# Kernel tuning notes

Measured on AMD Instinct MI355X. Metric: run time of the kernel, lower is better.

## Reference

```python
import jax, jax.numpy as jnp
import numpy as np

B, S, H, NH = 2, 2048, 1024, 16
HD = H // NH  # head_dim = 64


def setup_inputs() -> dict:
    key = jax.random.key(0)
    k1, k2, k3 = jax.random.split(key, 3)
    x = jax.random.normal(k1, (B, S, H), dtype=jnp.float32)
    # additive causal mask: 0 on/below diagonal, -1e9 above
    causal = jnp.tril(jnp.ones((S, S), dtype=bool))
    mask = jnp.where(causal, 0.0, -1e9).astype(jnp.float32)[None, None, :, :]
    # fan-in scaled init like flax Dense default (lecun_normal)
    W_qkv = jax.random.normal(k2, (H, 3 * H), dtype=jnp.float32) / np.sqrt(H)
    W_out = jax.random.normal(k3, (H, H), dtype=jnp.float32) / np.sqrt(H)
    return {"x": x, "mask": mask, "W_qkv": W_qkv, "W_out": W_out}


def reference(x, mask, W_qkv, W_out):
    b, s, _ = x.shape
    qkv = jnp.einsum('bsh,hf->bsf', x, W_qkv)  # [B,S,3H]
    q, k, v = jnp.split(qkv, 3, axis=-1)
    q = q.reshape(b, s, NH, HD)
    k = k.reshape(b, s, NH, HD)
    v = v.reshape(b, s, NH, HD)
    scores = jnp.einsum('bqhd,bkhd->bhqk', q, k) / jnp.sqrt(jnp.float32(HD))
    scores = scores + mask
    attn = jax.nn.softmax(scores, axis=-1)
    y = jnp.einsum('bhqk,bkhd->bqhd', attn, v).reshape(b, s, H)
    return jnp.einsum('bsh,ho->bso', y, W_out)
```

## Files before the change

### kernel.cpp

```cpp
#include <hip/hip_runtime.h>

#define B_ 2
#define S_ 2048
#define H_ 1024
#define NH_ 16
#define HD_ 64

typedef short s16x8 __attribute__((ext_vector_type(8)));
typedef float f32x4 __attribute__((ext_vector_type(4)));

__device__ __forceinline__ ushort f2bf(float f) {
  union { float f; unsigned u; } v;
  v.f = f;
  unsigned r = (v.u + 0x7fffu + ((v.u >> 16) & 1u)) >> 16;
  return (ushort)r;
}

__device__ __forceinline__ void gload16(const void* g, void* l) {
  typedef const __attribute__((address_space(1))) unsigned int* gp_t;
  typedef __attribute__((address_space(3))) unsigned int* lp_t;
  __builtin_amdgcn_global_load_lds((gp_t)g, (lp_t)l, 16, 0, 0);
}

__global__ __launch_bounds__(256) void k_prep(const float* __restrict__ x,
                                              ushort* __restrict__ xb,
                                              const float* __restrict__ Wqkv,
                                              ushort* __restrict__ wqkvT,
                                              const float* __restrict__ Wout,
                                              ushort* __restrict__ woutT) {
  __shared__ ushort tile[32][33];
  const int bid = blockIdx.x;
  if (bid < 4096) {
    int i = bid * 256 + threadIdx.x;
    float4 v = ((const float4*)x)[i];
    ushort4 o;
    o.x = f2bf(v.x); o.y = f2bf(v.y); o.z = f2bf(v.z); o.w = f2bf(v.w);
    ((ushort4*)xb)[i] = o;
    return;
  }
  const float* in;
  ushort* out;
  int R = 1024, C, t;
  if (bid < 7168) { in = Wqkv; out = wqkvT; C = 3072; t = bid - 4096; }
  else            { in = Wout; out = woutT; C = 1024; t = bid - 7168; }
  int nbx = C >> 5;
  int c0 = (t % nbx) * 32, r0 = (t / nbx) * 32;
  int tr = threadIdx.x >> 5, tc = threadIdx.x & 31;
#pragma unroll
  for (int i = 0; i < 4; ++i)
    tile[tr + 8 * i][tc] = f2bf(in[(size_t)(r0 + tr + 8 * i) * C + c0 + tc]);
  __syncthreads();
#pragma unroll
  for (int i = 0; i < 4; ++i)
    out[(size_t)(c0 + tr + 8 * i) * R + r0 + tc] = tile[tc][tr + 8 * i];
}

template <int MODE>
__global__ __launch_bounds__(512, 2) void k_gemm(const ushort* __restrict__ A,
                                                 const ushort* __restrict__ Bt,
                                                 void* __restrict__ out0,
                                                 ushort* __restrict__ outK,
                                                 ushort* __restrict__ outV,
                                                 int Kdim, int Ndim) {
  __shared__ __align__(16) ushort As[2][256 * 64];
  __shared__ __align__(16) ushort Bs[2][256 * 64];
  const int nwg = gridDim.x * gridDim.y;
  const int id = blockIdx.y * gridDim.x + blockIdx.x;
  const int sid = (id & 7) * (nwg >> 3) + (id >> 3);
  const int m0 = (sid / gridDim.x) * 256, n0 = (sid % gridDim.x) * 256;
  const int tid = threadIdx.x, lane = tid & 63, w = tid >> 6;
  const int g = lane >> 4, c = lane & 15;
  const int wm = w >> 2, wn = w & 3;
  f32x4 acc[8][4] = {};

  const int srow = tid >> 3;
  const int csrc = (tid & 7) ^ (srow & 7);
  const ushort* ag = A + (size_t)(m0 + srow) * Kdim + csrc * 8;
  const ushort* bg = Bt + (size_t)(n0 + srow) * Kdim + csrc * 8;
  const int nT = Kdim >> 6;

#define STRIPE(gp, ro, T_, dst) \
  gload16((gp) + (size_t)(ro) * Kdim + (T_) * 64, (dst) + tid * 8)

  STRIPE(ag, 0, 0, As[0]); STRIPE(ag, 64, 0, As[0] + 4096);
  STRIPE(bg, 0, 0, Bs[0]); STRIPE(bg, 64, 0, Bs[0] + 4096);
  STRIPE(bg, 128, 0, Bs[0] + 8192); STRIPE(bg, 192, 0, Bs[0] + 12288);
  STRIPE(ag, 128, 0, As[0] + 8192); STRIPE(ag, 192, 0, As[0] + 12288);
  asm volatile("s_waitcnt vmcnt(4)" ::: "memory");
  __builtin_amdgcn_s_barrier();
  __builtin_amdgcn_sched_barrier(0);

#pragma unroll 1
  for (int t = 0; t < nT; ++t) {
    const char* Ab = (const char*)As[t & 1];
    const char* Bb = (const char*)Bs[t & 1];
    const bool stg = (t + 1 < nT);
    const int T2 = t + 1, bf2 = T2 & 1;
#pragma unroll
    for (int q = 0; q < 4; ++q) {
      const int ih = q >> 1, jh = q & 1;
      s16x8 af[4][2], bfr[2][2];
#pragma unroll
      for (int i2 = 0; i2 < 4; ++i2) {
        int row = ih * 128 + wm * 64 + i2 * 16 + c;
#pragma unroll
        for (int kk = 0; kk < 2; ++kk) {
          int ch = g + kk * 4;
          af[i2][kk] = *(const s16x8*)(Ab + row * 128 + ((ch ^ (row & 7)) << 4));
        }
      }
#pragma unroll
      for (int j2 = 0; j2 < 2; ++j2) {
        int row = jh * 128 + wn * 32 + j2 * 16 + c;
#pragma unroll
        for (int kk = 0; kk < 2; ++kk) {
          int ch = g + kk * 4;
          bfr[j2][kk] = *(const s16x8*)(Bb + row * 128 + ((ch ^ (row & 7)) << 4));
        }
      }
      if (stg) {
        if (q == 0) { STRIPE(ag, 0, T2, As[bf2]);          STRIPE(ag, 64, T2, As[bf2] + 4096); }
        if (q == 1) { STRIPE(bg, 0, T2, Bs[bf2]);          STRIPE(bg, 64, T2, Bs[bf2] + 4096); }
        if (q == 2) { STRIPE(bg, 128, T2, Bs[bf2] + 8192); STRIPE(bg, 192, T2, Bs[bf2] + 12288); }
        if (q == 3) { STRIPE(ag, 128, T2, As[bf2] + 8192); STRIPE(ag, 192, T2, As[bf2] + 12288); }
      }
      __builtin_amdgcn_s_barrier();
      asm volatile("s_waitcnt lgkmcnt(0)" ::: "memory");
      __builtin_amdgcn_sched_barrier(0);
      __builtin_amdgcn_s_setprio(1);
#pragma unroll
      for (int i2 = 0; i2 < 4; ++i2)
#pragma unroll
        for (int j2 = 0; j2 < 2; ++j2)
#pragma unroll
          for (int kk = 0; kk < 2; ++kk)
            acc[ih * 4 + i2][jh * 2 + j2] = __builtin_amdgcn_mfma_f32_16x16x32_bf16(
                af[i2][kk], bfr[j2][kk], acc[ih * 4 + i2][jh * 2 + j2], 0, 0, 0);
      __builtin_amdgcn_s_setprio(0);
      if (stg) {
        if (q != 2) asm volatile("s_waitcnt vmcnt(4)" ::: "memory");
      } else {
        if (q == 0) asm volatile("s_waitcnt vmcnt(2)" ::: "memory");
        else if (q == 1) asm volatile("s_waitcnt vmcnt(0)" ::: "memory");
      }
      __builtin_amdgcn_s_barrier();
      __builtin_amdgcn_sched_barrier(0);
    }
  }
#undef STRIPE

  if (MODE == 1) {
    float* out = (float*)out0;
#pragma unroll
    for (int i = 0; i < 8; ++i) {
      int mb = m0 + (i >> 2) * 128 + wm * 64 + (i & 3) * 16 + g * 4;
#pragma unroll
      for (int j = 0; j < 4; ++j) {
        int n = n0 + (j >> 1) * 128 + wn * 32 + (j & 1) * 16 + c;
#pragma unroll
        for (int r = 0; r < 4; ++r)
          out[(size_t)(mb + r) * Ndim + n] = acc[i][j][r];
      }
    }
  } else {
    if (n0 < 1024) {
      const float ALPHA = 0.18033688f;
      ushort* outQ = (ushort*)out0;
#pragma unroll
      for (int i = 0; i < 8; ++i) {
        int mb = m0 + (i >> 2) * 128 + wm * 64 + (i & 3) * 16 + g * 4;
#pragma unroll
        for (int j = 0; j < 4; ++j) {
          int n = n0 + (j >> 1) * 128 + wn * 32 + (j & 1) * 16 + c;
#pragma unroll
          for (int r = 0; r < 4; ++r)
            outQ[(size_t)(mb + r) * 1024 + n] = f2bf(acc[i][j][r] * ALPHA);
        }
      }
    } else if (n0 < 2048) {
#pragma unroll
      for (int i = 0; i < 8; ++i) {
        int mb = m0 + (i >> 2) * 128 + wm * 64 + (i & 3) * 16 + g * 4;
#pragma unroll
        for (int j = 0; j < 4; ++j) {
          int n = n0 - 1024 + (j >> 1) * 128 + wn * 32 + (j & 1) * 16 + c;
#pragma unroll
          for (int r = 0; r < 4; ++r)
            outK[(size_t)(mb + r) * 1024 + n] = f2bf(acc[i][j][r]);
        }
      }
    } else {
#pragma unroll
      for (int i = 0; i < 8; ++i) {
        int mb = m0 + (i >> 2) * 128 + wm * 64 + (i & 3) * 16 + g * 4;
        int bidx = mb >> 11;
        int s = mb & 2047;
#pragma unroll
        for (int j = 0; j < 4; ++j) {
          int nv = n0 - 2048 + (j >> 1) * 128 + wn * 32 + (j & 1) * 16 + c;
          int h = nv >> 6, d = nv & 63;
          ushort4 pk;
          pk.x = f2bf(acc[i][j][0]);
          pk.y = f2bf(acc[i][j][1]);
          pk.z = f2bf(acc[i][j][2]);
          pk.w = f2bf(acc[i][j][3]);
          *(ushort4*)(outV + ((size_t)((bidx * 16 + h) * 64 + d)) * 2048 + s) = pk;
        }
      }
    }
  }
}

__global__ __launch_bounds__(256) void k_attn(const ushort* __restrict__ Qb,
                                              const ushort* __restrict__ Kb,
                                              const ushort* __restrict__ Vt,
                                              ushort* __restrict__ Yb) {
  __shared__ __align__(16) ushort Ks[2][64 * 64];
  __shared__ __align__(16) ushort Vs[2][64 * 64];
  __shared__ __align__(16) unsigned int Pp[4][16 * 32];
  const int fid = blockIdx.x;
  const int wid = (fid & 7) * 64 + (fid >> 3);
  const int bh = wid >> 4;
  const int j = wid & 15;
  const int b = bh >> 4, h = bh & 15;
  const int tid = threadIdx.x, w = tid >> 6, lane = tid & 63;
  const int g = lane >> 4, c = lane & 15;
  char* pb = (char*)(&Pp[w][0]);

  const int trow = tid >> 3, tcol = tid & 7;
  const int csrc = tcol ^ (trow & 7);
  const ushort* kgb = Kb + (size_t)(b * S_ + trow) * H_ + h * HD_ + csrc * 8;
  const ushort* vgb = Vt + (size_t)(bh * HD_ + trow) * S_ + csrc * 8;

#define STAGE(bf, tile)                                          \
  do {                                                           \
    int ks_ = (tile) * 64;                                       \
    gload16(kgb + (size_t)ks_ * H_, Ks[bf] + tid * 8);           \
    gload16(kgb + (size_t)(ks_ + 32) * H_, Ks[bf] + 2048 + tid * 8); \
    gload16(vgb + ks_, Vs[bf] + tid * 8);                        \
    gload16(vgb + ks_ + 32 * S_, Vs[bf] + 2048 + tid * 8);       \
  } while (0)

#pragma unroll 1
  for (int half = 0; half < 2; ++half) {
    const int qc = half ? (31 - j) : j;
    const int q0 = qc * 64;
    const int nt = qc + 1;
    const int qw = q0 + w * 16;

    s16x8 qf[2];
#pragma unroll
    for (int dc = 0; dc < 2; ++dc)
      qf[dc] = *(const s16x8*)(Qb + (size_t)(b * S_ + qw + c) * H_ +
                               h * HD_ + dc * 32 + g * 8);

    f32x4 oacc[4] = {};
    float m = -1e30f, lp = 0.f;

    STAGE(0, 0);
    asm volatile("s_waitcnt vmcnt(0)" ::: "memory");
    __builtin_amdgcn_s_barrier();
    __builtin_amdgcn_sched_barrier(0);

    int buf = 0;
#pragma unroll 1
    for (int it = 0; it < nt; ++it) {
      const int ks = it * 64;
      if (it + 1 < nt) STAGE(buf ^ 1, it + 1);

      f32x4 sacc[4] = {};
      __builtin_amdgcn_s_setprio(1);
#pragma unroll
      for (int dc = 0; dc < 2; ++dc) {
#pragma unroll
        for (int kt = 0; kt < 4; ++kt) {
          int R = kt * 16 + c;
          int cc = dc * 4 + g;
          s16x8 kf = *(const s16x8*)((const char*)Ks[buf] + R * 128 + ((cc ^ (R & 7)) << 4));
          sacc[kt] = __builtin_amdgcn_mfma_f32_16x16x32_bf16(kf, qf[dc], sacc[kt], 0, 0, 0);
        }
      }
      __builtin_amdgcn_s_setprio(0);

      if (it == nt - 1) {
        int q = qw + c;
#pragma unroll
        for (int kt = 0; kt < 4; ++kt)
#pragma unroll
          for (int r = 0; r < 4; ++r)
            if (ks + kt * 16 + g * 4 + r > q) sacc[kt][r] = -1e30f;
      }

      float t0 = fmaxf(fmaxf(sacc[0][0], sacc[0][1]), fmaxf(sacc[0][2], sacc[0][3]));
      float t1 = fmaxf(fmaxf(sacc[1][0], sacc[1][1]), fmaxf(sacc[1][2], sacc[1][3]));
      float t2 = fmaxf(fmaxf(sacc[2][0], sacc[2][1]), fmaxf(sacc[2][2], sacc[2][3]));
      float t3 = fmaxf(fmaxf(sacc[3][0], sacc[3][1]), fmaxf(sacc[3][2], sacc[3][3]));
      float t = fmaxf(fmaxf(t0, t1), fmaxf(t2, t3));
      t = fmaxf(t, __shfl_xor(t, 16));
      t = fmaxf(t, __shfl_xor(t, 32));

      if (__any(t > m + 8.0f)) {
        float mnew = fmaxf(m, t);
        float sc = __builtin_amdgcn_exp2f(m - mnew);
        m = mnew;
        lp *= sc;
        float scq[4];
#pragma unroll
        for (int r = 0; r < 4; ++r) scq[r] = __shfl(sc, g * 4 + r);
#pragma unroll
        for (int dt = 0; dt < 4; ++dt)
#pragma unroll
          for (int r = 0; r < 4; ++r) oacc[dt][r] *= scq[r];
      }

      float p[4][4];
      float rs = 0.f;
#pragma unroll
      for (int kt = 0; kt < 4; ++kt)
#pragma unroll
        for (int r = 0; r < 4; ++r) {
          p[kt][r] = __builtin_amdgcn_exp2f(sacc[kt][r] - m);
          rs += p[kt][r];
        }
      lp += rs;
      unsigned int pw[8];
#pragma unroll
      for (int kt = 0; kt < 4; ++kt) {
        asm("v_cvt_pk_bf16_f32 %0, %1, %2" : "=v"(pw[kt * 2 + 0]) : "v"(p[kt][0]), "v"(p[kt][1]));
        asm("v_cvt_pk_bf16_f32 %0, %1, %2" : "=v"(pw[kt * 2 + 1]) : "v"(p[kt][2]), "v"(p[kt][3]));
      }
#pragma unroll
      for (int kt = 0; kt < 4; ++kt) {
        int qd = kt * 2 + (g >> 1);
        *(uint2*)(pb + c * 128 + ((qd ^ (c & 7)) << 4) + ((g & 1) << 3)) =
            make_uint2(pw[kt * 2], pw[kt * 2 + 1]);
      }
      asm volatile("s_waitcnt lgkmcnt(0)" ::: "memory");
      __builtin_amdgcn_sched_barrier(0);

      __builtin_amdgcn_s_setprio(1);
#pragma unroll
      for (int kc = 0; kc < 2; ++kc) {
        int qd = kc * 4 + g;
        s16x8 pf = *(const s16x8*)(pb + c * 128 + ((qd ^ (c & 7)) << 4));
        int cc = kc * 4 + g;
#pragma unroll
        for (int dt = 0; dt < 4; ++dt) {
          int R = dt * 16 + c;
          s16x8 vf = *(const s16x8*)((const char*)Vs[buf] + R * 128 + ((cc ^ (R & 7)) << 4));
          oacc[dt] = __builtin_amdgcn_mfma_f32_16x16x32_bf16(pf, vf, oacc[dt], 0, 0, 0);
        }
      }
      __builtin_amdgcn_s_setprio(0);

      asm volatile("s_waitcnt vmcnt(0)" ::: "memory");
      __builtin_amdgcn_s_barrier();
      __builtin_amdgcn_sched_barrier(0);
      buf ^= 1;
    }

    float lt = lp;
    lt += __shfl_xor(lt, 16);
    lt += __shfl_xor(lt, 32);
    float rq[4];
#pragma unroll
    for (int r = 0; r < 4; ++r) rq[r] = 1.0f / __shfl(lt, g * 4 + r);
#pragma unroll
    for (int dt = 0; dt < 4; ++dt)
#pragma unroll
      for (int r = 0; r < 4; ++r) {
        int s = qw + g * 4 + r;
        Yb[(size_t)(b * S_ + s) * H_ + h * HD_ + dt * 16 + c] = f2bf(oacc[dt][r] * rq[r]);
      }
  }
#undef STAGE
}

extern "C" void kernel_launch(void* const* d_in, const int* in_sizes, int n_in,
                              void* d_out, int out_size, void* d_ws, size_t ws_size,
                              hipStream_t stream) {
  (void)in_sizes; (void)n_in; (void)out_size; (void)ws_size;
  const float* x = (const float*)d_in[0];
  const float* Wqkv = (const float*)d_in[2];
  const float* Wout = (const float*)d_in[3];
  float* out = (float*)d_out;

  char* ws = (char*)d_ws;
  ushort* xb    = (ushort*)(ws + 0);
  ushort* wqkvT = (ushort*)(ws + 8388608);
  ushort* woutT = (ushort*)(ws + 14680064);
  ushort* Qb    = (ushort*)(ws + 16777216);
  ushort* Kb    = (ushort*)(ws + 25165824);
  ushort* Vtb   = (ushort*)(ws + 33554432);
  ushort* Yb    = (ushort*)(ws + 41943040);

  k_prep<<<dim3(8192), dim3(256), 0, stream>>>(x, xb, Wqkv, wqkvT, Wout, woutT);
  k_gemm<0><<<dim3(12, 16), dim3(512), 0, stream>>>(xb, wqkvT, (void*)Qb, Kb, Vtb, 1024, 3072);
  k_attn<<<dim3(512), dim3(256), 0, stream>>>(Qb, Kb, Vtb, Yb);
  k_gemm<1><<<dim3(4, 16), dim3(512), 0, stream>>>(Yb, woutT, (void*)out, nullptr, nullptr, 1024, 1024);
}
```

Before: 214.2 us.

## Split attention into 32-row query blocks and add 128x128 output-projection GEMM kernel

The attention kernel now uses 128-thread blocks with two waves, each covering a 32-row query chunk, and launches 1024 blocks instead of 512. This raises the workgroup count so more of the GPU's compute units stay busy under the causal imbalance. The output projection moves from the 256x256-tile GEMM (only 64 workgroups) to a new 128x128-tile kernel launched with 256 workgroups, for better occupancy on a small GEMM. The cost is that each K/V tile is loaded by more workgroups, and the new GEMM uses a simpler double-buffered pipeline with a full vmcnt(0) wait on every step.

```diff
diff --git a/kernel.cpp b/kernel.cpp
--- a/kernel.cpp
+++ b/kernel.cpp
@@ -149,20 +149,7 @@
   }
 #undef STRIPE
 
-  if (MODE == 1) {
-    float* out = (float*)out0;
-#pragma unroll
-    for (int i = 0; i < 8; ++i) {
-      int mb = m0 + (i >> 2) * 128 + wm * 64 + (i & 3) * 16 + g * 4;
-#pragma unroll
-      for (int j = 0; j < 4; ++j) {
-        int n = n0 + (j >> 1) * 128 + wn * 32 + (j & 1) * 16 + c;
-#pragma unroll
-        for (int r = 0; r < 4; ++r)
-          out[(size_t)(mb + r) * Ndim + n] = acc[i][j][r];
-      }
-    }
-  } else {
+  {
     if (n0 < 1024) {
       const float ALPHA = 0.18033688f;
       ushort* outQ = (ushort*)out0;
@@ -211,17 +198,90 @@
   }
 }
 
-__global__ __launch_bounds__(256) void k_attn(const ushort* __restrict__ Qb,
+__global__ __launch_bounds__(256) void k_gemm_o(const ushort* __restrict__ A,
+                                                const ushort* __restrict__ Bt,
+                                                float* __restrict__ out,
+                                                int Kdim, int Ndim) {
+  __shared__ __align__(16) ushort As[2][128 * 64];
+  __shared__ __align__(16) ushort Bs[2][128 * 64];
+  const int nwg = gridDim.x * gridDim.y;
+  const int id = blockIdx.y * gridDim.x + blockIdx.x;
+  const int sid = (id & 7) * (nwg >> 3) + (id >> 3);
+  const int m0 = (sid / gridDim.x) * 128, n0 = (sid % gridDim.x) * 128;
+  const int tid = threadIdx.x, lane = tid & 63, w = tid >> 6;
+  const int g = lane >> 4, c = lane & 15;
+  const int wr = w >> 1, wc = w & 1;
+  f32x4 acc[4][4] = {};
+  const int trow = tid >> 3, tcol = tid & 7;
+  const ushort* ag = A + (size_t)(m0 + trow) * Kdim + tcol * 8;
+  const ushort* bg = Bt + (size_t)(n0 + trow) * Kdim + tcol * 8;
+
+#define STG_O(bf, k0)                                        \
+  do {                                                       \
+    _Pragma("unroll") for (int i_ = 0; i_ < 4; ++i_) {       \
+      gload16(ag + (k0) + i_ * 32 * Kdim, As[bf] + tid * 8 + i_ * 2048); \
+      gload16(bg + (k0) + i_ * 32 * Kdim, Bs[bf] + tid * 8 + i_ * 2048); \
+    }                                                        \
+  } while (0)
+
+  const int nk = Kdim >> 6;
+  STG_O(0, 0);
+  asm volatile("s_waitcnt vmcnt(0)" ::: "memory");
+  __builtin_amdgcn_s_barrier();
+  __builtin_amdgcn_sched_barrier(0);
+
+  int buf = 0;
+#pragma unroll 1
+  for (int t = 0; t < nk; ++t) {
+    if (t + 1 < nk) STG_O(buf ^ 1, (t + 1) * 64);
+#pragma unroll
+    for (int kk = 0; kk < 64; kk += 32) {
+      s16x8 af[4], bfr[4];
+#pragma unroll
+      for (int i = 0; i < 4; ++i)
+        af[i] = *(const s16x8*)(As[buf] + (wr * 64 + i * 16 + c) * 64 + kk + g * 8);
+#pragma unroll
+      for (int i = 0; i < 4; ++i)
+        bfr[i] = *(const s16x8*)(Bs[buf] + (wc * 64 + i * 16 + c) * 64 + kk + g * 8);
+      __builtin_amdgcn_s_setprio(1);
+#pragma unroll
+      for (int i = 0; i < 4; ++i)
+#pragma unroll
+        for (int j = 0; j < 4; ++j)
+          acc[i][j] = __builtin_amdgcn_mfma_f32_16x16x32_bf16(af[i], bfr[j], acc[i][j], 0, 0, 0);
+      __builtin_amdgcn_s_setprio(0);
+    }
+    asm volatile("s_waitcnt vmcnt(0)" ::: "memory");
+    __builtin_amdgcn_s_barrier();
+    __builtin_amdgcn_sched_barrier(0);
+    buf ^= 1;
+  }
+#undef STG_O
+
+#pragma unroll
+  for (int i = 0; i < 4; ++i) {
+    int mb = m0 + wr * 64 + i * 16 + g * 4;
+#pragma unroll
+    for (int j = 0; j < 4; ++j) {
+      int n = n0 + wc * 64 + j * 16 + c;
+#pragma unroll
+      for (int r = 0; r < 4; ++r)
+        out[(size_t)(mb + r) * Ndim + n] = acc[i][j][r];
+    }
+  }
+}
+
+__global__ __launch_bounds__(128) void k_attn(const ushort* __restrict__ Qb,
                                               const ushort* __restrict__ Kb,
                                               const ushort* __restrict__ Vt,
                                               ushort* __restrict__ Yb) {
   __shared__ __align__(16) ushort Ks[2][64 * 64];
   __shared__ __align__(16) ushort Vs[2][64 * 64];
-  __shared__ __align__(16) unsigned int Pp[4][16 * 32];
+  __shared__ __align__(16) unsigned int Pp[2][16 * 32];
   const int fid = blockIdx.x;
-  const int wid = (fid & 7) * 64 + (fid >> 3);
-  const int bh = wid >> 4;
-  const int j = wid & 15;
+  const int wid = (fid & 7) * 128 + (fid >> 3);
+  const int bh = wid >> 5;
+  const int j = wid & 31;
   const int b = bh >> 4, h = bh & 15;
   const int tid = threadIdx.x, w = tid >> 6, lane = tid & 63;
   const int g = lane >> 4, c = lane & 15;
@@ -232,20 +292,24 @@
   const ushort* kgb = Kb + (size_t)(b * S_ + trow) * H_ + h * HD_ + csrc * 8;
   const ushort* vgb = Vt + (size_t)(bh * HD_ + trow) * S_ + csrc * 8;
 
-#define STAGE(bf, tile)                                          \
-  do {                                                           \
-    int ks_ = (tile) * 64;                                       \
-    gload16(kgb + (size_t)ks_ * H_, Ks[bf] + tid * 8);           \
+#define STAGE(bf, tile)                                              \
+  do {                                                               \
+    int ks_ = (tile) * 64;                                           \
+    gload16(kgb + (size_t)(ks_ +  0) * H_, Ks[bf] +    0 + tid * 8); \
+    gload16(kgb + (size_t)(ks_ + 16) * H_, Ks[bf] + 1024 + tid * 8); \
     gload16(kgb + (size_t)(ks_ + 32) * H_, Ks[bf] + 2048 + tid * 8); \
-    gload16(vgb + ks_, Vs[bf] + tid * 8);                        \
-    gload16(vgb + ks_ + 32 * S_, Vs[bf] + 2048 + tid * 8);       \
+    gload16(kgb + (size_t)(ks_ + 48) * H_, Ks[bf] + 3072 + tid * 8); \
+    gload16(vgb + ks_ +  0 * S_, Vs[bf] +    0 + tid * 8);           \
+    gload16(vgb + ks_ + 16 * S_, Vs[bf] + 1024 + tid * 8);           \
+    gload16(vgb + ks_ + 32 * S_, Vs[bf] + 2048 + tid * 8);           \
+    gload16(vgb + ks_ + 48 * S_, Vs[bf] + 3072 + tid * 8);           \
   } while (0)
 
 #pragma unroll 1
   for (int half = 0; half < 2; ++half) {
-    const int qc = half ? (31 - j) : j;
-    const int q0 = qc * 64;
-    const int nt = qc + 1;
+    const int qc = half ? (63 - j) : j;
+    const int q0 = qc * 32;
+    const int nt = (qc >> 1) + 1;
     const int qw = q0 + w * 16;
 
     s16x8 qf[2];
@@ -396,6 +460,6 @@
 
   k_prep<<<dim3(8192), dim3(256), 0, stream>>>(x, xb, Wqkv, wqkvT, Wout, woutT);
   k_gemm<0><<<dim3(12, 16), dim3(512), 0, stream>>>(xb, wqkvT, (void*)Qb, Kb, Vtb, 1024, 3072);
-  k_attn<<<dim3(512), dim3(256), 0, stream>>>(Qb, Kb, Vtb, Yb);
-  k_gemm<1><<<dim3(4, 16), dim3(512), 0, stream>>>(Yb, woutT, (void*)out, nullptr, nullptr, 1024, 1024);
-}
+  k_attn<<<dim3(1024), dim3(128), 0, stream>>>(Qb, Kb, Vtb, Yb);
+  k_gemm_o<<<dim3(8, 32), dim3(256), 0, stream>>>(Yb, woutT, out, 1024, 1024);
+}
```

New measurement: 204.9 us. 4.3% less time.
